# Optimization experiments

Measured on AMD Instinct MI355X. Metric: run time of the kernel, lower is better.

The kernel has to match this reference:

```python
import jax, jax.numpy as jnp
import numpy as np

N = 200000
K = 16
D = 32
IN_SIZE = K * (K - 1) // 2  # 120
HID = 128


def setup_inputs() -> dict:
    key = jax.random.key(0)
    ks = jax.random.split(key, 12)
    E = N * K
    x = jax.random.normal(ks[0], (N, D), dtype=jnp.float32)
    edge_attr = jax.random.normal(ks[1], (E, D), dtype=jnp.float32)
    # kNN-style edge_index: source node i owns edges [i*K, (i+1)*K)
    src = jnp.repeat(jnp.arange(N, dtype=jnp.int64), K)
    dst = jax.random.randint(ks[2], (E,), 0, N, dtype=jnp.int64)
    edge_index = jnp.stack([src, dst], axis=0)
    s = 0.1
    W1 = jax.random.normal(ks[3], (IN_SIZE, HID), dtype=jnp.float32) * s
    b1 = jnp.zeros((HID,), dtype=jnp.float32)
    W2 = jax.random.normal(ks[4], (HID, HID), dtype=jnp.float32) * s
    b2 = jnp.zeros((HID,), dtype=jnp.float32)
    W3 = jax.random.normal(ks[5], (HID, HID), dtype=jnp.float32) * s
    b3 = jnp.zeros((HID,), dtype=jnp.float32)
    W4 = jax.random.normal(ks[6], (HID, 1), dtype=jnp.float32) * s
    b4 = jnp.zeros((1,), dtype=jnp.float32)
    return {"x": x, "edge_index": edge_index, "edge_attr": edge_attr, "k": K,
            "W1": W1, "b1": b1, "W2": W2, "b2": b2, "W3": W3, "b3": b3,
            "W4": W4, "b4": b4}


def calc_pair_angles(edge_attr, k):
    # edge_attr: [N*k, d] per-edge neighbor vectors, grouped k per node
    E, d = edge_attr.shape
    n = E // k
    v = edge_attr.reshape(n, k, d)
    vn = v / (jnp.linalg.norm(v, axis=-1, keepdims=True) + 1e-12)
    cos = jnp.einsum('nkd,nmd->nkm', vn, vn)  # [n, k, k]
    cos = jnp.clip(cos, -1.0 + 1e-7, 1.0 - 1e-7)
    ang = jnp.arccos(cos)
    iu, ju = jnp.triu_indices(k, 1)
    return ang[:, iu, ju]  # [n, k*(k-1)/2]


def reference(x, edge_index, edge_attr, k, W1, b1, W2, b2, W3, b3, W4, b4):
    # message() returns edge_attr; aggregate() computes pairwise neighbor angles
    feats = calc_pair_angles(edge_attr, k)  # [N, 120]
    h = jnp.tanh(feats @ W1 + b1)
    h = jnp.tanh(h @ W2 + b2)
    h = jnp.tanh(h @ W3 + b3)
    out = jax.nn.sigmoid(h @ W4 + b4)  # [N, 1]
    return out[:, 0]  # squeeze, [N]
```

## Files before the change

### kernel.cpp

```cpp
#include <hip/hip_runtime.h>
#include <hip/hip_bf16.h>
#include <math.h>


#define NTHREADS 256
#define CHUNK    16
#define ASTRIDE  136
#define PBLOCKS  512

typedef _Float16 f16;
typedef f16  f16x8 __attribute__((ext_vector_type(8)));
typedef f16  f16x4 __attribute__((ext_vector_type(4)));
typedef float f32x4 __attribute__((ext_vector_type(4)));

#define MFMA16(a, b, c) __builtin_amdgcn_mfma_f32_16x16x32_f16(a, b, c, 0, 0, 0)

__device__ __forceinline__ float fast_tanh(float x) {
    float e = __expf(2.0f * x);
    return 1.0f - 2.0f * __builtin_amdgcn_rcpf(e + 1.0f);
}

__device__ __forceinline__ float fast_acos(float x) {
    float ax = fabsf(x);
    float p = fmaf(-0.0187293f, ax, 0.0742610f);
    p = fmaf(p, ax, -0.2121144f);
    p = fmaf(p, ax, 1.5707288f);
    float r = sqrtf(1.0f - ax) * p;
    return (x >= 0.0f) ? r : (3.14159265358979f - r);
}

__device__ __forceinline__ void load_lds16(const float* g, float* l) {
    __builtin_amdgcn_global_load_lds(
        (__attribute__((address_space(1))) void*)(g),
        (__attribute__((address_space(3))) void*)(l), 16, 0, 0);
}

__global__ void prep_weights(const float* __restrict__ W1,
                             const float* __restrict__ W2,
                             const float* __restrict__ W3,
                             f16* __restrict__ wt)
{
    int tid = blockIdx.x * 256 + threadIdx.x;
    if (tid >= 3 * 128 * 128) return;
    int layer = tid >> 14;
    int rem   = tid & 16383;
    int j     = rem >> 7;
    int i     = rem & 127;
    const float* W = (layer == 0) ? W1 : ((layer == 1) ? W2 : W3);
    int in_l = (layer == 0) ? 120 : 128;
    float v = (i < in_l) ? W[i * 128 + j] : 0.0f;
    wt[tid] = (f16)v;
}

__global__ __launch_bounds__(NTHREADS, 2)
void gnn_pipe(const float* __restrict__ edge_attr,
              const f16*   __restrict__ wt,
              const float* __restrict__ b1, const float* __restrict__ b2,
              const float* __restrict__ b3,
              const float* __restrict__ W4, const float* __restrict__ b4,
              float* __restrict__ out, int n_nodes, int nchunks)
{
    __shared__ __attribute__((aligned(16))) float stg[2][8192];
    __shared__ __attribute__((aligned(16))) f16   actA[16 * ASTRIDE];
    __shared__ __attribute__((aligned(16))) f16   actB[16 * ASTRIDE];
    __shared__ __attribute__((aligned(16))) float diag[4][4][16];

    const int t  = threadIdx.x;
    const int w  = t >> 6;
    const int l  = t & 63;
    const int lr = l & 15;
    const int lg = l >> 4;

    if (t < 128) actA[(t >> 3) * ASTRIDE + 120 + (t & 7)] = (f16)0.f;

    #define LW(L, jj, kt) (*(const f16x8*)(wt + (L) * 16384 + ((w * 2 + (jj)) * 16 + lr) * 128 + (kt) * 32 + lg * 8))
    const f16x8 W000 = LW(0,0,0), W001 = LW(0,0,1), W002 = LW(0,0,2), W003 = LW(0,0,3);
    const f16x8 W010 = LW(0,1,0), W011 = LW(0,1,1), W012 = LW(0,1,2), W013 = LW(0,1,3);
    const f16x8 W100 = LW(1,0,0), W101 = LW(1,0,1), W102 = LW(1,0,2), W103 = LW(1,0,3);
    const f16x8 W110 = LW(1,1,0), W111 = LW(1,1,1), W112 = LW(1,1,2), W113 = LW(1,1,3);
    const f16x8 W200 = LW(2,0,0), W201 = LW(2,0,1), W202 = LW(2,0,2), W203 = LW(2,0,3);
    const f16x8 W210 = LW(2,1,0), W211 = LW(2,1,1), W212 = LW(2,1,2), W213 = LW(2,1,3);
    #undef LW
    const f32x4 bva0 = *(const f32x4*)(b1 + (w * 2 + 0) * 16 + lg * 4);
    const f32x4 bva1 = *(const f32x4*)(b1 + (w * 2 + 1) * 16 + lg * 4);
    const f32x4 bvb0 = *(const f32x4*)(b2 + (w * 2 + 0) * 16 + lg * 4);
    const f32x4 bvb1 = *(const f32x4*)(b2 + (w * 2 + 1) * 16 + lg * 4);
    const f32x4 bvc0 = *(const f32x4*)(b3 + (w * 2 + 0) * 16 + lg * 4);
    const f32x4 bvc1 = *(const f32x4*)(b3 + (w * 2 + 1) * 16 + lg * 4);
    const int   fpart = t & 15;
    const f32x4 w4a = *(const f32x4*)(W4 + fpart * 8);
    const f32x4 w4b = *(const f32x4*)(W4 + fpart * 8 + 4);
    const float bb4 = b4[0];

    const int swsrc = (l * 16) ^ ((l >> 3) << 4);

    #define STAGE(ch_, b_)                                                       \
        {                                                                        \
            const long n0_ = (long)(ch_) * CHUNK + w * 4;                        \
            _Pragma("unroll")                                                    \
            for (int i_ = 0; i_ < 8; ++i_) {                                     \
                long nd_ = n0_ + (i_ >> 1);                                      \
                if (nd_ >= n_nodes) nd_ = n_nodes - 1;                           \
                const float* gs_ = (const float*)((const char*)edge_attr         \
                                   + nd_ * 2048 + (i_ & 1) * 1024 + swsrc);      \
                load_lds16(gs_, &stg[b_][w * 2048 + i_ * 256]);                  \
            }                                                                    \
        }

    #define LBAR()                                                               \
        {                                                                        \
            asm volatile("s_waitcnt lgkmcnt(0)" ::: "memory");                   \
            __builtin_amdgcn_s_barrier();                                        \
            __builtin_amdgcn_sched_barrier(0);                                   \
        }

    #define LAYER(SRC, DST, Wa0, Wa1, Wa2, Wa3, Wb0, Wb1, Wb2, Wb3, BV0, BV1)   \
        {                                                                        \
            const f16* sr_ = SRC + lr * ASTRIDE + lg * 8;                        \
            f16x8 s0_ = *(const f16x8*)(sr_);                                    \
            f16x8 s1_ = *(const f16x8*)(sr_ + 32);                               \
            f16x8 s2_ = *(const f16x8*)(sr_ + 64);                               \
            f16x8 s3_ = *(const f16x8*)(sr_ + 96);                               \
            f32x4 a0_ = {0.f, 0.f, 0.f, 0.f}, a1_ = a0_;                         \
            a0_ = MFMA16(Wa0, s0_, a0_); a1_ = MFMA16(Wb0, s0_, a1_);            \
            a0_ = MFMA16(Wa1, s1_, a0_); a1_ = MFMA16(Wb1, s1_, a1_);            \
            a0_ = MFMA16(Wa2, s2_, a0_); a1_ = MFMA16(Wb2, s2_, a1_);            \
            a0_ = MFMA16(Wa3, s3_, a0_); a1_ = MFMA16(Wb3, s3_, a1_);            \
            f16x4 o0_, o1_;                                                      \
            _Pragma("unroll")                                                    \
            for (int r_ = 0; r_ < 4; ++r_) {                                     \
                o0_[r_] = (f16)fast_tanh(a0_[r_] + BV0[r_]);                     \
                o1_[r_] = (f16)fast_tanh(a1_[r_] + BV1[r_]);                     \
            }                                                                    \
            *(f16x4*)(DST + lr * ASTRIDE + (w * 2 + 0) * 16 + lg * 4) = o0_;     \
            *(f16x4*)(DST + lr * ASTRIDE + (w * 2 + 1) * 16 + lg * 4) = o1_;     \
        }

    long ch = blockIdx.x;
    STAGE(ch, 0);
    asm volatile("s_waitcnt vmcnt(0)" ::: "memory");
    __builtin_amdgcn_sched_barrier(0);

    int it = 0;
    for (; ch < nchunks; ch += PBLOCKS, ++it) {
        const int b = it & 1;
        if (it) {
            asm volatile("s_waitcnt vmcnt(1)" ::: "memory");
            __builtin_amdgcn_sched_barrier(0);
        }

        const char* ws_ = (const char*)&stg[b][w * 2048];
        const int abase = lr * 128 + lg * 32;
        const int akey  = (lr & 7) << 4;
        f16x8 f0, f1, f2, f3;
        #define FRAG(fc, m_)                                                     \
            {                                                                    \
                float4 va = *(const float4*)(ws_ + (m_) * 2048 + (abase ^ akey));        \
                float4 vb = *(const float4*)(ws_ + (m_) * 2048 + ((abase + 16) ^ akey)); \
                fc[0]=(f16)va.x; fc[1]=(f16)va.y; fc[2]=(f16)va.z; fc[3]=(f16)va.w;      \
                fc[4]=(f16)vb.x; fc[5]=(f16)vb.y; fc[6]=(f16)vb.z; fc[7]=(f16)vb.w;      \
            }
        FRAG(f0, 0) FRAG(f1, 1) FRAG(f2, 2) FRAG(f3, 3)
        #undef FRAG

        const long nxt = ch + PBLOCKS;
        if (nxt < nchunks) STAGE(nxt, b ^ 1);

        f32x4 g0, g1, g2, g3;
        {
            f32x4 z = {0.f, 0.f, 0.f, 0.f};
            g0 = MFMA16(f0, f0, z); g1 = MFMA16(f1, f1, z);
            g2 = MFMA16(f2, f2, z); g3 = MFMA16(f3, f3, z);
        }
        if (lg == (lr >> 2)) {
            const int r = lr & 3;
            diag[w][0][lr] = __builtin_amdgcn_rsqf(g0[r] + 1e-24f);
            diag[w][1][lr] = __builtin_amdgcn_rsqf(g1[r] + 1e-24f);
            diag[w][2][lr] = __builtin_amdgcn_rsqf(g2[r] + 1e-24f);
            diag[w][3][lr] = __builtin_amdgcn_rsqf(g3[r] + 1e-24f);
        }
        asm volatile("s_waitcnt lgkmcnt(0)" ::: "memory");
        __builtin_amdgcn_sched_barrier(0);

        #define FIN(gc, c)                                                       \
            {                                                                    \
                const float rc = diag[w][c][lr];                                 \
                const f32x4 rr = *(const f32x4*)&diag[w][c][lg * 4];             \
                const int m_ = w * 4 + (c);                                      \
                const int col = lr;                                              \
                _Pragma("unroll")                                                \
                for (int r2 = 0; r2 < 4; ++r2) {                                 \
                    const int row = lg * 4 + r2;                                 \
                    float cv = gc[r2] * rr[r2] * rc;                             \
                    cv = fminf(fmaxf(cv, -1.0f + 1e-7f), 1.0f - 1e-7f);          \
                    float ang = fast_acos(cv);                                   \
                    if (row < col) {                                             \
                        const int p = 15*row - ((row*(row-1))>>1) + (col-row-1); \
                        actA[m_ * ASTRIDE + p] = (f16)ang;                       \
                    }                                                            \
                }                                                                \
            }
        FIN(g0, 0) FIN(g1, 1) FIN(g2, 2) FIN(g3, 3)
        #undef FIN

        LBAR();

        LAYER(actA, actB, W000, W001, W002, W003, W010, W011, W012, W013, bva0, bva1);
        LBAR();
        LAYER(actB, actA, W100, W101, W102, W103, W110, W111, W112, W113, bvb0, bvb1);
        LBAR();
        LAYER(actA, actB, W200, W201, W202, W203, W210, W211, W212, W213, bvc0, bvc1);
        LBAR();

        {
            const int node_ = t >> 4;
            const f16* fs_ = actB + node_ * ASTRIDE + fpart * 8;
            f16x8 h_ = *(const f16x8*)(fs_);
            float s_ = 0.f;
            s_ = fmaf((float)h_[0], w4a[0], s_); s_ = fmaf((float)h_[1], w4a[1], s_);
            s_ = fmaf((float)h_[2], w4a[2], s_); s_ = fmaf((float)h_[3], w4a[3], s_);
            s_ = fmaf((float)h_[4], w4b[0], s_); s_ = fmaf((float)h_[5], w4b[1], s_);
            s_ = fmaf((float)h_[6], w4b[2], s_); s_ = fmaf((float)h_[7], w4b[3], s_);
            s_ += __shfl_xor(s_, 1);
            s_ += __shfl_xor(s_, 2);
            s_ += __shfl_xor(s_, 4);
            s_ += __shfl_xor(s_, 8);
            if (fpart == 0) {
                const long gn_ = ch * CHUNK + node_;
                if (gn_ < n_nodes)
                    out[gn_] = __builtin_amdgcn_rcpf(1.0f + __expf(-(s_ + bb4)));
            }
        }
    }
    #undef STAGE
    #undef LBAR
    #undef LAYER
}

extern "C" void kernel_launch(void* const* d_in, const int* in_sizes, int n_in,
                              void* d_out, int out_size, void* d_ws, size_t ws_size,
                              hipStream_t stream) {
    const float* edge_attr = (const float*)d_in[2];
    const float* W1 = (const float*)d_in[4];
    const float* b1 = (const float*)d_in[5];
    const float* W2 = (const float*)d_in[6];
    const float* b2 = (const float*)d_in[7];
    const float* W3 = (const float*)d_in[8];
    const float* b3 = (const float*)d_in[9];
    const float* W4 = (const float*)d_in[10];
    const float* b4 = (const float*)d_in[11];
    float* out = (float*)d_out;
    f16* wt = (f16*)d_ws;

    const int n_nodes = in_sizes[2] / 512;
    const int nchunks = (n_nodes + CHUNK - 1) / CHUNK;
    const int blocks  = PBLOCKS < nchunks ? PBLOCKS : nchunks;

    prep_weights<<<(3 * 128 * 128 + 255) / 256, 256, 0, stream>>>(W1, W2, W3, wt);

    gnn_pipe<<<blocks, NTHREADS, 0, stream>>>(
        edge_attr, wt, b1, b2, b3, W4, b4, out, n_nodes, nchunks);
}
```

Measured before the change: 130.5 us.

## Software-pipeline angle front-end of next chunk with MLP layers of current chunk

```diff
diff --git a/kernel.cpp b/kernel.cpp
--- a/kernel.cpp
+++ b/kernel.cpp
@@ -53,17 +53,19 @@
 }
 
 __global__ __launch_bounds__(NTHREADS, 2)
-void gnn_pipe(const float* __restrict__ edge_attr,
-              const f16*   __restrict__ wt,
-              const float* __restrict__ b1, const float* __restrict__ b2,
-              const float* __restrict__ b3,
-              const float* __restrict__ W4, const float* __restrict__ b4,
-              float* __restrict__ out, int n_nodes, int nchunks)
+void gnn_pipe2(const float* __restrict__ edge_attr,
+               const f16*   __restrict__ wt,
+               const float* __restrict__ b1, const float* __restrict__ b2,
+               const float* __restrict__ b3,
+               const float* __restrict__ W4, const float* __restrict__ b4,
+               float* __restrict__ out, int n_nodes, int nchunks)
 {
     __shared__ __attribute__((aligned(16))) float stg[2][8192];
-    __shared__ __attribute__((aligned(16))) f16   actA[16 * ASTRIDE];
-    __shared__ __attribute__((aligned(16))) f16   actB[16 * ASTRIDE];
+    __shared__ __attribute__((aligned(16))) f16   actX0[16 * ASTRIDE];
+    __shared__ __attribute__((aligned(16))) f16   actX1[16 * ASTRIDE];
+    __shared__ __attribute__((aligned(16))) f16   actY [16 * ASTRIDE];
     __shared__ __attribute__((aligned(16))) float diag[4][4][16];
+    __shared__ __attribute__((aligned(16))) float pbuf[16][4];
 
     const int t  = threadIdx.x;
     const int w  = t >> 6;
@@ -71,7 +73,8 @@
     const int lr = l & 15;
     const int lg = l >> 4;
 
-    if (t < 128) actA[(t >> 3) * ASTRIDE + 120 + (t & 7)] = (f16)0.f;
+    if (t < 128)       actX0[(t >> 3) * ASTRIDE + 120 + (t & 7)] = (f16)0.f;
+    else               actX1[((t - 128) >> 3) * ASTRIDE + 120 + (t & 7)] = (f16)0.f;
 
     #define LW(L, jj, kt) (*(const f16x8*)(wt + (L) * 16384 + ((w * 2 + (jj)) * 16 + lr) * 128 + (kt) * 32 + lg * 8))
     const f16x8 W000 = LW(0,0,0), W001 = LW(0,0,1), W002 = LW(0,0,2), W003 = LW(0,0,3);
@@ -87,10 +90,9 @@
     const f32x4 bvb1 = *(const f32x4*)(b2 + (w * 2 + 1) * 16 + lg * 4);
     const f32x4 bvc0 = *(const f32x4*)(b3 + (w * 2 + 0) * 16 + lg * 4);
     const f32x4 bvc1 = *(const f32x4*)(b3 + (w * 2 + 1) * 16 + lg * 4);
-    const int   fpart = t & 15;
-    const f32x4 w4a = *(const f32x4*)(W4 + fpart * 8);
-    const f32x4 w4b = *(const f32x4*)(W4 + fpart * 8 + 4);
-    const float bb4 = b4[0];
+    const f32x4 w4v0 = *(const f32x4*)(W4 + w * 32 + lg * 4);
+    const f32x4 w4v1 = *(const f32x4*)(W4 + w * 32 + 16 + lg * 4);
+    const float bb4  = b4[0];
 
     const int swsrc = (l * 16) ^ ((l >> 3) << 4);
 
@@ -114,9 +116,58 @@
             __builtin_amdgcn_sched_barrier(0);                                   \
         }
 
+    #define AFRONT(b_)                                                           \
+        {                                                                        \
+            const char* ws_ = (const char*)&stg[b_][w * 2048];                   \
+            const int abase = lr * 128 + lg * 32;                                \
+            const int akey  = (lr & 7) << 4;                                     \
+            f16x8 f0, f1, f2, f3;                                                \
+            _FR(f0, 0) _FR(f1, 1) _FR(f2, 2) _FR(f3, 3)                          \
+            f32x4 z_ = {0.f, 0.f, 0.f, 0.f};                                     \
+            g0 = MFMA16(f0, f0, z_); g1 = MFMA16(f1, f1, z_);                    \
+            g2 = MFMA16(f2, f2, z_); g3 = MFMA16(f3, f3, z_);                    \
+            if (lg == (lr >> 2)) {                                               \
+                const int r_ = lr & 3;                                           \
+                diag[w][0][lr] = __builtin_amdgcn_rsqf(g0[r_] + 1e-24f);         \
+                diag[w][1][lr] = __builtin_amdgcn_rsqf(g1[r_] + 1e-24f);         \
+                diag[w][2][lr] = __builtin_amdgcn_rsqf(g2[r_] + 1e-24f);         \
+                diag[w][3][lr] = __builtin_amdgcn_rsqf(g3[r_] + 1e-24f);         \
+            }                                                                    \
+        }
+    #define _FR(fc, m_)                                                          \
+        {                                                                        \
+            float4 va = *(const float4*)(ws_ + (m_) * 2048 + (abase ^ akey));        \
+            float4 vb = *(const float4*)(ws_ + (m_) * 2048 + ((abase + 16) ^ akey)); \
+            fc[0]=(f16)va.x; fc[1]=(f16)va.y; fc[2]=(f16)va.z; fc[3]=(f16)va.w;      \
+            fc[4]=(f16)vb.x; fc[5]=(f16)vb.y; fc[6]=(f16)vb.z; fc[7]=(f16)vb.w;      \
+        }
+
+    #define FINX(DST)                                                            \
+        {                                                                        \
+            _FN(g0, 0, DST) _FN(g1, 1, DST) _FN(g2, 2, DST) _FN(g3, 3, DST)      \
+        }
+    #define _FN(gc, c_, DST)                                                     \
+        {                                                                        \
+            const float rc = diag[w][c_][lr];                                    \
+            const f32x4 rr = *(const f32x4*)&diag[w][c_][lg * 4];                \
+            const int m_ = w * 4 + (c_);                                         \
+            const int col = lr;                                                  \
+            _Pragma("unroll")                                                    \
+            for (int r2 = 0; r2 < 4; ++r2) {                                     \
+                const int row = lg * 4 + r2;                                     \
+                float cv = gc[r2] * rr[r2] * rc;                                 \
+                cv = fminf(fmaxf(cv, -1.0f + 1e-7f), 1.0f - 1e-7f);              \
+                float ang = fast_acos(cv);                                       \
+                if (row < col) {                                                 \
+                    const int p_ = 15*row - ((row*(row-1))>>1) + (col-row-1);    \
+                    (DST)[m_ * ASTRIDE + p_] = (f16)ang;                         \
+                }                                                                \
+            }                                                                    \
+        }
+
     #define LAYER(SRC, DST, Wa0, Wa1, Wa2, Wa3, Wb0, Wb1, Wb2, Wb3, BV0, BV1)   \
         {                                                                        \
-            const f16* sr_ = SRC + lr * ASTRIDE + lg * 8;                        \
+            const f16* sr_ = (SRC) + lr * ASTRIDE + lg * 8;                      \
             f16x8 s0_ = *(const f16x8*)(sr_);                                    \
             f16x8 s1_ = *(const f16x8*)(sr_ + 32);                               \
             f16x8 s2_ = *(const f16x8*)(sr_ + 64);                               \
@@ -132,109 +183,102 @@
                 o0_[r_] = (f16)fast_tanh(a0_[r_] + BV0[r_]);                     \
                 o1_[r_] = (f16)fast_tanh(a1_[r_] + BV1[r_]);                     \
             }                                                                    \
-            *(f16x4*)(DST + lr * ASTRIDE + (w * 2 + 0) * 16 + lg * 4) = o0_;     \
-            *(f16x4*)(DST + lr * ASTRIDE + (w * 2 + 1) * 16 + lg * 4) = o1_;     \
-        }
-
-    long ch = blockIdx.x;
-    STAGE(ch, 0);
+            *(f16x4*)((DST) + lr * ASTRIDE + (w * 2 + 0) * 16 + lg * 4) = o0_;   \
+            *(f16x4*)((DST) + lr * ASTRIDE + (w * 2 + 1) * 16 + lg * 4) = o1_;   \
+        }
+
+    #define LAYER3(SRC)                                                          \
+        {                                                                        \
+            const f16* sr_ = (SRC) + lr * ASTRIDE + lg * 8;                      \
+            f16x8 s0_ = *(const f16x8*)(sr_);                                    \
+            f16x8 s1_ = *(const f16x8*)(sr_ + 32);                               \
+            f16x8 s2_ = *(const f16x8*)(sr_ + 64);                               \
+            f16x8 s3_ = *(const f16x8*)(sr_ + 96);                               \
+            f32x4 a0_ = {0.f, 0.f, 0.f, 0.f}, a1_ = a0_;                         \
+            a0_ = MFMA16(W200, s0_, a0_); a1_ = MFMA16(W210, s0_, a1_);          \
+            a0_ = MFMA16(W201, s1_, a0_); a1_ = MFMA16(W211, s1_, a1_);          \
+            a0_ = MFMA16(W202, s2_, a0_); a1_ = MFMA16(W212, s2_, a1_);          \
+            a0_ = MFMA16(W203, s3_, a0_); a1_ = MFMA16(W213, s3_, a1_);          \
+            float p_ = 0.f;                                                      \
+            _Pragma("unroll")                                                    \
+            for (int r_ = 0; r_ < 4; ++r_) {                                     \
+                p_ = fmaf(fast_tanh(a0_[r_] + bvc0[r_]), w4v0[r_], p_);          \
+                p_ = fmaf(fast_tanh(a1_[r_] + bvc1[r_]), w4v1[r_], p_);          \
+            }                                                                    \
+            p_ += __shfl_xor(p_, 16);                                            \
+            p_ += __shfl_xor(p_, 32);                                            \
+            if (l < 16) pbuf[lr][w] = p_;                                        \
+        }
+
+    #define FINALSUM(ch_)                                                        \
+        {                                                                        \
+            if (t < 16) {                                                        \
+                f32x4 pv_ = *(const f32x4*)&pbuf[t][0];                          \
+                float s_ = (pv_[0] + pv_[1]) + (pv_[2] + pv_[3]);                \
+                const long gn_ = (long)(ch_) * CHUNK + t;                        \
+                if (gn_ < n_nodes)                                               \
+                    out[gn_] = __builtin_amdgcn_rcpf(1.0f + __expf(-(s_ + bb4)));\
+            }                                                                    \
+        }
+
+    const long c0 = blockIdx.x;
+    const int  K  = (int)((nchunks - c0 + PBLOCKS - 1) / PBLOCKS);
+
+    f32x4 g0, g1, g2, g3;
+
+    STAGE(c0, 0);
     asm volatile("s_waitcnt vmcnt(0)" ::: "memory");
     __builtin_amdgcn_sched_barrier(0);
-
-    int it = 0;
-    for (; ch < nchunks; ch += PBLOCKS, ++it) {
-        const int b = it & 1;
-        if (it) {
-            asm volatile("s_waitcnt vmcnt(1)" ::: "memory");
+    AFRONT(0);
+    asm volatile("s_waitcnt lgkmcnt(0)" ::: "memory");
+    __builtin_amdgcn_sched_barrier(0);
+    FINX(actX0);
+    if (K > 1) STAGE(c0 + PBLOCKS, 1);
+    LBAR();
+
+    f16* Xcur = actX0;
+    f16* Xnxt = actX1;
+    int  bufn = 1;
+
+    for (int k = 0; k < K; ++k) {
+        const long cc   = c0 + (long)k * PBLOCKS;
+        const bool hasN = (k + 1 < K);
+
+        LAYER(Xcur, actY, W000, W001, W002, W003, W010, W011, W012, W013, bva0, bva1);
+        if (k > 0) FINALSUM(cc - PBLOCKS);
+        if (hasN) {
+            if (k == 0) { asm volatile("s_waitcnt vmcnt(0)" ::: "memory"); }
+            else        { asm volatile("s_waitcnt vmcnt(1)" ::: "memory"); }
             __builtin_amdgcn_sched_barrier(0);
-        }
-
-        const char* ws_ = (const char*)&stg[b][w * 2048];
-        const int abase = lr * 128 + lg * 32;
-        const int akey  = (lr & 7) << 4;
-        f16x8 f0, f1, f2, f3;
-        #define FRAG(fc, m_)                                                     \
-            {                                                                    \
-                float4 va = *(const float4*)(ws_ + (m_) * 2048 + (abase ^ akey));        \
-                float4 vb = *(const float4*)(ws_ + (m_) * 2048 + ((abase + 16) ^ akey)); \
-                fc[0]=(f16)va.x; fc[1]=(f16)va.y; fc[2]=(f16)va.z; fc[3]=(f16)va.w;      \
-                fc[4]=(f16)vb.x; fc[5]=(f16)vb.y; fc[6]=(f16)vb.z; fc[7]=(f16)vb.w;      \
-            }
-        FRAG(f0, 0) FRAG(f1, 1) FRAG(f2, 2) FRAG(f3, 3)
-        #undef FRAG
-
-        const long nxt = ch + PBLOCKS;
-        if (nxt < nchunks) STAGE(nxt, b ^ 1);
-
-        f32x4 g0, g1, g2, g3;
-        {
-            f32x4 z = {0.f, 0.f, 0.f, 0.f};
-            g0 = MFMA16(f0, f0, z); g1 = MFMA16(f1, f1, z);
-            g2 = MFMA16(f2, f2, z); g3 = MFMA16(f3, f3, z);
-        }
-        if (lg == (lr >> 2)) {
-            const int r = lr & 3;
-            diag[w][0][lr] = __builtin_amdgcn_rsqf(g0[r] + 1e-24f);
-            diag[w][1][lr] = __builtin_amdgcn_rsqf(g1[r] + 1e-24f);
-            diag[w][2][lr] = __builtin_amdgcn_rsqf(g2[r] + 1e-24f);
-            diag[w][3][lr] = __builtin_amdgcn_rsqf(g3[r] + 1e-24f);
-        }
-        asm volatile("s_waitcnt lgkmcnt(0)" ::: "memory");
-        __builtin_amdgcn_sched_barrier(0);
-
-        #define FIN(gc, c)                                                       \
-            {                                                                    \
-                const float rc = diag[w][c][lr];                                 \
-                const f32x4 rr = *(const f32x4*)&diag[w][c][lg * 4];             \
-                const int m_ = w * 4 + (c);                                      \
-                const int col = lr;                                              \
-                _Pragma("unroll")                                                \
-                for (int r2 = 0; r2 < 4; ++r2) {                                 \
-                    const int row = lg * 4 + r2;                                 \
-                    float cv = gc[r2] * rr[r2] * rc;                             \
-                    cv = fminf(fmaxf(cv, -1.0f + 1e-7f), 1.0f - 1e-7f);          \
-                    float ang = fast_acos(cv);                                   \
-                    if (row < col) {                                             \
-                        const int p = 15*row - ((row*(row-1))>>1) + (col-row-1); \
-                        actA[m_ * ASTRIDE + p] = (f16)ang;                       \
-                    }                                                            \
-                }                                                                \
-            }
-        FIN(g0, 0) FIN(g1, 1) FIN(g2, 2) FIN(g3, 3)
-        #undef FIN
-
+            AFRONT(bufn);
+        }
         LBAR();
 
-        LAYER(actA, actB, W000, W001, W002, W003, W010, W011, W012, W013, bva0, bva1);
+        LAYER(actY, Xcur, W100, W101, W102, W103, W110, W111, W112, W113, bvb0, bvb1);
+        if (hasN) {
+            FINX(Xnxt);
+            if (k + 2 < K) STAGE(cc + 2 * PBLOCKS, bufn ^ 1);
+        }
         LBAR();
-        LAYER(actB, actA, W100, W101, W102, W103, W110, W111, W112, W113, bvb0, bvb1);
+
+        LAYER3(Xcur);
         LBAR();
-        LAYER(actA, actB, W200, W201, W202, W203, W210, W211, W212, W213, bvc0, bvc1);
-        LBAR();
-
-        {
-            const int node_ = t >> 4;
-            const f16* fs_ = actB + node_ * ASTRIDE + fpart * 8;
-            f16x8 h_ = *(const f16x8*)(fs_);
-            float s_ = 0.f;
-            s_ = fmaf((float)h_[0], w4a[0], s_); s_ = fmaf((float)h_[1], w4a[1], s_);
-            s_ = fmaf((float)h_[2], w4a[2], s_); s_ = fmaf((float)h_[3], w4a[3], s_);
-            s_ = fmaf((float)h_[4], w4b[0], s_); s_ = fmaf((float)h_[5], w4b[1], s_);
-            s_ = fmaf((float)h_[6], w4b[2], s_); s_ = fmaf((float)h_[7], w4b[3], s_);
-            s_ += __shfl_xor(s_, 1);
-            s_ += __shfl_xor(s_, 2);
-            s_ += __shfl_xor(s_, 4);
-            s_ += __shfl_xor(s_, 8);
-            if (fpart == 0) {
-                const long gn_ = ch * CHUNK + node_;
-                if (gn_ < n_nodes)
-                    out[gn_] = __builtin_amdgcn_rcpf(1.0f + __expf(-(s_ + bb4)));
-            }
-        }
+
+        f16* tmp = Xcur; Xcur = Xnxt; Xnxt = tmp;
+        bufn ^= 1;
     }
+
+    FINALSUM(c0 + (long)(K - 1) * PBLOCKS);
+
     #undef STAGE
     #undef LBAR
+    #undef AFRONT
+    #undef _FR
+    #undef FINX
+    #undef _FN
     #undef LAYER
+    #undef LAYER3
+    #undef FINALSUM
 }
 
 extern "C" void kernel_launch(void* const* d_in, const int* in_sizes, int n_in,
@@ -258,6 +302,6 @@
 
     prep_weights<<<(3 * 128 * 128 + 255) / 256, 256, 0, stream>>>(W1, W2, W3, wt);
 
-    gnn_pipe<<<blocks, NTHREADS, 0, stream>>>(
+    gnn_pipe2<<<blocks, NTHREADS, 0, stream>>>(
         edge_attr, wt, b1, b2, b3, W4, b4, out, n_nodes, nchunks);
 }
```

After: 138.2 us. 6.0% more time.
